# Optimization experiments

Measured on AMD Instinct MI355X. Metric: run time of the kernel, lower is better.

## Reference

```python
import jax, jax.numpy as jnp
import numpy as np

INPUT_SIZE = 416
NUM_CLASSES = 80
A = 3  # anchors per yolo layer
SS = [13, 26, 52]  # grid sizes (strides 32/16/8)
ANCHORS = [[(116, 90), (156, 198), (373, 326)],
           [(30, 61), (62, 45), (59, 119)],
           [(10, 13), (16, 30), (33, 23)]]
B, L = 16, 50


def _build_priors():
    boxes, cols, rows, pws, phs, szs = [], [], [], [], [], []
    for l, S in enumerate(SS):
        for i in range(S):
            for j in range(S):
                cx, cy = (j + 0.5) / S, (i + 0.5) / S
                for (aw, ah) in ANCHORS[l]:
                    w, h = aw / INPUT_SIZE, ah / INPUT_SIZE
                    boxes.append((cx - 0.5 * w, cy - 0.5 * h, w, h))
                    cols.append(j); rows.append(i)
                    pws.append(aw); phs.append(ah); szs.append(S)
    f = lambda a: np.asarray(a, np.float32)
    return f(boxes), f(cols), f(rows), f(pws), f(phs), f(szs)

PRIORS_NP, PCOL_NP, PROW_NP, PPW_NP, PPH_NP, PS_NP = _build_priors()
N = PRIORS_NP.shape[0]  # 10647
OFF = np.concatenate([[0], np.cumsum([S * S * A for S in SS])])


def setup_inputs() -> dict:
    key = jax.random.key(0)
    ks = jax.random.split(key, 8)
    inp = {}
    for l, S in enumerate(SS):
        inp[f"yolo_out{l}"] = jax.random.normal(ks[l], (B, A * (NUM_CLASSES + 5), S, S), jnp.float32)
    cls = jax.random.randint(ks[3], (B, L), 0, NUM_CLASSES).astype(jnp.float32)
    valid = jax.random.uniform(ks[4], (B, L)) < 0.4
    cls = jnp.where(valid, cls, -1.0)  # class < 0 means padding label
    xy = jax.random.uniform(ks[5], (B, L, 2), minval=0.0, maxval=0.7)
    wh = jax.random.uniform(ks[6], (B, L, 2), minval=0.05, maxval=0.3)
    inp["labels"] = jnp.concatenate([cls[..., None], xy, wh], axis=-1)[:, None]  # [B,1,L,5]
    return inp


def _bce(p, t):
    # torch BCELoss (mean) with the same log clamp at -100
    lg = lambda x: jnp.maximum(jnp.log(x), -100.0)
    return jnp.mean(-(t * lg(p) + (1.0 - t) * lg(1.0 - p)))


def _build_targets(labels):
    pri = jnp.asarray(PRIORS_NP)
    lab = labels[:, 0]  # [B,L,5]
    cls = lab[..., 0]
    valid = cls >= 0.0  # [B,L]
    bx, by, bw, bh = lab[..., 1], lab[..., 2], lab[..., 3], lab[..., 4]
    px, py, pw, ph = pri[:, 0], pri[:, 1], pri[:, 2], pri[:, 3]
    # IoU of every label against every prior: [B,L,N]
    ix = jnp.maximum(px, bx[..., None]); iy = jnp.maximum(py, by[..., None])
    ax = jnp.minimum(px + pw, (bx + bw)[..., None]); ay = jnp.minimum(py + ph, (by + bh)[..., None])
    inter = jnp.maximum(ax - ix, 0.0) * jnp.maximum(ay - iy, 0.0)
    ious = inter / (pw * ph + (bw * bh)[..., None] - inter)

    # priors with IoU>=0.5 to any gt are ignored for objectness (unless chosen as best)
    suppressed = jnp.any((ious >= 0.5) & valid[..., None], axis=1)  # [B,N]

    # best prior per label; on ties, pick the middle tied index (as the original)
    m = jnp.max(ious, axis=-1, keepdims=True)
    tie = ious == m
    k = tie.sum(-1)
    rank = (k - 1) // 2 + 1
    cs = jnp.cumsum(tie, -1)
    idx = jnp.argmax(tie & (cs == rank[..., None]), axis=-1)  # [B,L]

    colc = jnp.asarray(PCOL_NP)[idx]; rowc = jnp.asarray(PROW_NP)[idx]
    pwc = jnp.asarray(PPW_NP)[idx]; phc = jnp.asarray(PPH_NP)[idx]
    Sc = jnp.asarray(PS_NP)[idx]
    dx = jnp.clip((bx + 0.5 * bw) * Sc - colc, 1e-6, 0.999999)
    dy = jnp.clip((by + 0.5 * bh) * Sc - rowc, 1e-6, 0.999999)
    t_all = jnp.stack([jnp.log(dx / (1.0 - dx)), jnp.log(dy / (1.0 - dy)),
                       jnp.log(bw * INPUT_SIZE / pwc), jnp.log(bh * INPUT_SIZE / phc)], -1)  # [B,L,4]

    flat = (jnp.arange(B)[:, None] * N + idx).reshape(-1)  # [B*L]
    vflat = valid.reshape(-1)
    g = jnp.arange(B * L)
    winner = jax.ops.segment_max(jnp.where(vflat, g, -1), flat, num_segments=B * N)
    chosen = winner >= 0  # [B*N]
    coord_t = jnp.where(chosen[:, None], t_all.reshape(-1, 4)[jnp.clip(winner, 0)], 0.0)

    cls_i = jnp.where(vflat, cls.reshape(-1).astype(jnp.int32), 0)
    class_t = jnp.zeros((B * N, NUM_CLASSES), jnp.float32).at[flat, cls_i].max(vflat.astype(jnp.float32))

    obj_t = chosen.astype(jnp.float32).reshape(B, N)
    obj_m = (chosen.reshape(B, N) | ~suppressed).astype(jnp.float32)
    pos_m = chosen.astype(jnp.float32).reshape(B, N)
    return jax.lax.stop_gradient(
        (obj_t, obj_m, pos_m, coord_t.reshape(B, N, 4), class_t.reshape(B, N, NUM_CLASSES)))


def reference(yolo_out0, yolo_out1, yolo_out2, labels):
    obj_t, obj_m, pos_m, coord_t, class_t = _build_targets(labels)
    outs = [yolo_out0, yolo_out1, yolo_out2]
    Cp5 = NUM_CLASSES + 5
    obj_loss = coord_loss = class_loss = 0.0
    for l, S in enumerate(SS):
        n0, n1 = int(OFF[l]), int(OFF[l + 1])
        out = outs[l]
        # per-prior ordering within a layer is (row, col, anchor)
        om = obj_m[:, n0:n1].reshape(B, S, S, A).transpose(0, 3, 1, 2)
        ot = obj_t[:, n0:n1].reshape(B, S, S, A).transpose(0, 3, 1, 2)
        pm = pos_m[:, n0:n1].reshape(B, S, S, A)
        ct = coord_t[:, n0:n1].reshape(B, S, S, A, 4).transpose(0, 3, 4, 1, 2).reshape(B, A * 4, S, S)
        cm = jnp.broadcast_to(pm[..., None], (B, S, S, A, 4)).transpose(0, 3, 4, 1, 2).reshape(B, A * 4, S, S)
        kt = class_t[:, n0:n1].reshape(B, S, S, A, NUM_CLASSES).transpose(0, 3, 4, 1, 2).reshape(B, A * NUM_CLASSES, S, S)
        km = jnp.broadcast_to(pm[..., None], (B, S, S, A, NUM_CLASSES)).transpose(0, 3, 4, 1, 2).reshape(B, A * NUM_CLASSES, S, S)
        oi = np.arange(A) * Cp5 + 4
        ci = (np.arange(A)[:, None] * Cp5 + np.arange(4)).reshape(-1)
        ki = (np.arange(A)[:, None] * Cp5 + 5 + np.arange(NUM_CLASSES)).reshape(-1)
        obj_loss = obj_loss + _bce(jax.nn.sigmoid(out[:, oi]) * om, ot * om)
        coord_loss = coord_loss + jnp.mean((out[:, ci] * cm - ct * cm) ** 2)
        class_loss = class_loss + _bce(jax.nn.sigmoid(out[:, ki]) * km, kt * km)
    return jnp.stack([obj_loss, coord_loss, class_loss])
```

## Files before the change

### kernel.cpp

```cpp
#include <hip/hip_runtime.h>

#define NPRI 10647
#define BB 16
#define LL 50
#define OBJ_BLOCKS 666
#define CHO_BLOCKS (BB * LL)
#define TOT_BLOCKS (OBJ_BLOCKS + CHO_BLOCKS)

__device__ __constant__ double c_hw[3][3] = {
    {0.5*(116.0/416.0), 0.5*(156.0/416.0), 0.5*(373.0/416.0)},
    {0.5*( 30.0/416.0), 0.5*( 62.0/416.0), 0.5*( 59.0/416.0)},
    {0.5*( 10.0/416.0), 0.5*( 16.0/416.0), 0.5*( 33.0/416.0)}};
__device__ __constant__ double c_hh[3][3] = {
    {0.5*( 90.0/416.0), 0.5*(198.0/416.0), 0.5*(326.0/416.0)},
    {0.5*( 61.0/416.0), 0.5*( 45.0/416.0), 0.5*(119.0/416.0)},
    {0.5*( 23.0/416.0), 0.5*( 30.0/416.0), 0.5*( 23.0/416.0)}};
__device__ __constant__ float c_pwf[3][3] = {
    {(float)(116.0/416.0), (float)(156.0/416.0), (float)(373.0/416.0)},
    {(float)( 30.0/416.0), (float)( 62.0/416.0), (float)( 59.0/416.0)},
    {(float)( 10.0/416.0), (float)( 16.0/416.0), (float)( 33.0/416.0)}};
__device__ __constant__ float c_phf[3][3] = {
    {(float)( 90.0/416.0), (float)(198.0/416.0), (float)(326.0/416.0)},
    {(float)( 61.0/416.0), (float)( 45.0/416.0), (float)(119.0/416.0)},
    {(float)( 23.0/416.0), (float)( 30.0/416.0), (float)( 23.0/416.0)}};
__device__ __constant__ float c_awf[3][3] = {{116,156,373},{30,62,59},{10,16,33}};
__device__ __constant__ float c_ahf[3][3] = {{90,198,326},{61,45,119},{23,30,23}};
__device__ __constant__ double c_wObj[3] = {1.0/8112.0, 1.0/32448.0, 1.0/129792.0};

__device__ inline void decode_prior(int n, int& level, int& S, int& ii, int& jj,
                                    int& aa, int& off) {
    if (n < 507)        { level = 0; S = 13; int c = n / 3;            aa = n - 3*c;            jj = c % 13; ii = c / 13; off = 0;  }
    else if (n < 2535)  { level = 1; S = 26; int nn = n - 507;  int c = nn / 3; aa = nn - 3*c; jj = c % 26; ii = c / 26; off = 13; }
    else                { level = 2; S = 52; int nn = n - 2535; int c = nn / 3; aa = nn - 3*c; jj = c % 52; ii = c / 52; off = 39; }
}

__global__ __launch_bounds__(256) void assign_kernel(
    const float* __restrict__ labels, int* __restrict__ idxArr,
    float4* __restrict__ tcoord) {
    __shared__ double s_cx[91];
    __shared__ float  s_iou[NPRI];
    __shared__ float  s_red[256];
    __shared__ int    s_cnt[256];

    int tid = threadIdx.x;
    int gi  = blockIdx.x;
    const float* lab = labels + gi * 5;
    float cls = lab[0];
    if (tid == 0) idxArr[gi] = -1;
    if (cls < 0.0f) return;

    if (tid < 91) {
        int S, idx;
        if (tid < 13)      { S = 13; idx = tid; }
        else if (tid < 39) { S = 26; idx = tid - 13; }
        else               { S = 52; idx = tid - 39; }
        s_cx[tid] = ((double)idx + 0.5) / (double)S;
    }

    float bx = lab[1], by = lab[2], bw = lab[3], bh = lab[4];
    float bxe  = __fadd_rn(bx, bw), bye = __fadd_rn(by, bh);
    float bwbh = __fmul_rn(bw, bh);
    __syncthreads();

    float lmax = -3.0e38f;
    for (int n = tid; n < NPRI; n += 256) {
        int level, S, ii, jj, aa, off;
        decode_prior(n, level, S, ii, jj, aa, off);
        float px  = (float)(s_cx[off + jj] - c_hw[level][aa]);
        float py  = (float)(s_cx[off + ii] - c_hh[level][aa]);
        float pwf = c_pwf[level][aa], phf = c_phf[level][aa];
        float pxe = __fadd_rn(px, pwf), pye = __fadd_rn(py, phf);
        float pwph = __fmul_rn(pwf, phf);
        float ix = fmaxf(px, bx), iy = fmaxf(py, by);
        float ax = fminf(pxe, bxe), ay = fminf(pye, bye);
        float iw = fmaxf(__fsub_rn(ax, ix), 0.0f);
        float ih = fmaxf(__fsub_rn(ay, iy), 0.0f);
        float inter = __fmul_rn(iw, ih);
        float denom = __fsub_rn(__fadd_rn(pwph, bwbh), inter);
        float iou = __fdiv_rn(inter, denom);
        s_iou[n] = iou;
        lmax = fmaxf(lmax, iou);
    }
    s_red[tid] = lmax;
    __syncthreads();
    for (int s = 128; s > 0; s >>= 1) {
        if (tid < s) s_red[tid] = fmaxf(s_red[tid], s_red[tid + s]);
        __syncthreads();
    }
    float m = s_red[0];

    const int CH = 42;
    int start = tid * CH;
    int end   = min(start + CH, NPRI);
    int cnt = 0;
    for (int n = start; n < end; ++n) cnt += (s_iou[n] == m) ? 1 : 0;

    s_cnt[tid] = cnt;
    __syncthreads();
    for (int d = 1; d < 256; d <<= 1) {
        int add = (tid >= d) ? s_cnt[tid - d] : 0;
        __syncthreads();
        s_cnt[tid] += add;
        __syncthreads();
    }
    int k    = s_cnt[255];
    int rank = (k - 1) / 2 + 1;
    int pre  = s_cnt[tid] - cnt;

    if (pre < rank && rank <= pre + cnt) {
        int r = rank - pre;
        int sel = -1;
        for (int n = start; n < end; ++n)
            if (s_iou[n] == m && --r == 0) { sel = n; break; }
        int level, S, ii, jj, aa, off;
        decode_prior(sel, level, S, ii, jj, aa, off);
        float Sf = (float)S, colf = (float)jj, rowf = (float)ii;
        float dx = __fsub_rn(__fmul_rn(__fadd_rn(bx, __fmul_rn(0.5f, bw)), Sf), colf);
        float dy = __fsub_rn(__fmul_rn(__fadd_rn(by, __fmul_rn(0.5f, bh)), Sf), rowf);
        dx = fminf(fmaxf(dx, 1e-6f), 0.999999f);
        dy = fminf(fmaxf(dy, 1e-6f), 0.999999f);
        float t0 = logf(__fdiv_rn(dx, __fsub_rn(1.0f, dx)));
        float t1 = logf(__fdiv_rn(dy, __fsub_rn(1.0f, dy)));
        float t2 = logf(__fdiv_rn(__fmul_rn(bw, 416.0f), c_awf[level][aa]));
        float t3 = logf(__fdiv_rn(__fmul_rn(bh, 416.0f), c_ahf[level][aa]));
        tcoord[gi] = make_float4(t0, t1, t2, t3);
        idxArr[gi] = sel;
    }
}

__global__ __launch_bounds__(256) void loss_kernel(
    const float* __restrict__ o0, const float* __restrict__ o1, const float* __restrict__ o2,
    const float* __restrict__ labels, const int* __restrict__ idxArr,
    const float4* __restrict__ tcoord,
    double* __restrict__ pObj, double* __restrict__ pCoord, double* __restrict__ pClass) {
    __shared__ float  s_box[2][LL][4];
    __shared__ float  s_cls[2][LL];
    __shared__ int    s_idx[2][LL];
    __shared__ double s_red[256];
    int tid = threadIdx.x;

    if (blockIdx.x < OBJ_BLOCKS) {
        int e0 = blockIdx.x * 256;
        int b0 = e0 / NPRI;
        int b1 = min((e0 + 255) / NPRI, BB - 1);
        for (int t = tid; t < 2 * LL; t += 256) {
            int which = t / LL, l = t - which * LL;
            int b = which ? b1 : b0;
            const float* lab = labels + (b * LL + l) * 5;
            s_cls[which][l]    = lab[0];
            s_box[which][l][0] = lab[1];
            s_box[which][l][1] = lab[2];
            s_box[which][l][2] = lab[3];
            s_box[which][l][3] = lab[4];
            s_idx[which][l]    = idxArr[b * LL + l];
        }
        __syncthreads();

        int e = e0 + tid;
        double a = 0.0;
        if (e < BB * NPRI) {
            int b = e / NPRI, n = e - b * NPRI;
            int which = (b == b0) ? 0 : 1;
            int level, S, ii, jj, aa, off;
            decode_prior(n, level, S, ii, jj, aa, off);
            double cxd = ((double)jj + 0.5) / (double)S;
            double cyd = ((double)ii + 0.5) / (double)S;
            float px  = (float)(cxd - c_hw[level][aa]);
            float py  = (float)(cyd - c_hh[level][aa]);
            float pwf = c_pwf[level][aa], phf = c_phf[level][aa];
            float pxe = __fadd_rn(px, pwf), pye = __fadd_rn(py, phf);
            float pwph = __fmul_rn(pwf, phf);
            bool supp = false, chosen = false;
            for (int l = 0; l < LL; ++l) {
                if (s_cls[which][l] < 0.0f) continue;
                if (s_idx[which][l] == n) chosen = true;
                float bx = s_box[which][l][0], by = s_box[which][l][1];
                float bw = s_box[which][l][2], bh = s_box[which][l][3];
                float ix = fmaxf(px, bx), iy = fmaxf(py, by);
                float ax = fminf(pxe, __fadd_rn(bx, bw));
                float ay = fminf(pye, __fadd_rn(by, bh));
                float iw = fmaxf(__fsub_rn(ax, ix), 0.0f);
                float ih = fmaxf(__fsub_rn(ay, iy), 0.0f);
                float inter = __fmul_rn(iw, ih);
                float denom = __fsub_rn(__fadd_rn(pwph, __fmul_rn(bw, bh)), inter);
                float iou = __fdiv_rn(inter, denom);
                if (iou >= 0.5f) supp = true;
            }
            if (chosen || !supp) {
                int SS2 = S * S;
                const float* out = (level == 0) ? o0 : ((level == 1) ? o1 : o2);
                float x = out[(size_t)b * 255 * SS2 + (aa * 85 + 4) * SS2 + ii * S + jj];
                float p = 1.0f / (1.0f + expf(-x));
                float t = chosen ? 1.0f : 0.0f;
                float lp = fmaxf(logf(p), -100.0f);
                float lq = fmaxf(logf(1.0f - p), -100.0f);
                a = -(double)(t * lp + (1.0f - t) * lq) * c_wObj[level];
            }
        }
        s_red[tid] = a; __syncthreads();
        for (int s = 128; s > 0; s >>= 1) { if (tid < s) s_red[tid] += s_red[tid + s]; __syncthreads(); }
        if (tid == 0) pObj[blockIdx.x] = s_red[0];
    } else {
        int gi = blockIdx.x - OBJ_BLOCKS;
        int b  = gi / LL, lsel = gi - b * LL;
        if (tid < LL) {
            s_idx[0][tid] = idxArr[b * LL + tid];
            s_cls[0][tid] = labels[(b * LL + tid) * 5];
        }
        __syncthreads();
        int sel = s_idx[0][lsel];
        int maxl = -1;
        if (sel >= 0)
            for (int l = 0; l < LL; ++l) if (s_idx[0][l] == sel) maxl = l;
        bool active = (sel >= 0) && (maxl == lsel);
        if (!active) {
            if (tid == 0) { pCoord[gi] = 0.0; pClass[gi] = 0.0; }
            return;
        }
        int level, S, ii, jj, aa, off;
        decode_prior(sel, level, S, ii, jj, aa, off);
        int SS2 = S * S;
        const float* out = (level == 0) ? o0 : ((level == 1) ? o1 : o2);
        const float* base = out + (size_t)b * 255 * SS2 + aa * 85 * SS2 + ii * S + jj;
        double wObj = c_wObj[level];

        double val = 0.0;
        if (tid < 4) {
            float4 ct = tcoord[gi];
            float ctk = (tid == 0) ? ct.x : (tid == 1) ? ct.y : (tid == 2) ? ct.z : ct.w;
            float x = base[tid * SS2];
            float d = __fsub_rn(x, ctk);
            val = (double)__fmul_rn(d, d) * (wObj * 0.25);
        } else if (tid >= 5 && tid < 85) {
            int cc = tid - 5;
            float x = base[tid * SS2];
            float t = 0.0f;
            for (int l = 0; l < LL; ++l)
                if (s_idx[0][l] == sel && (int)s_cls[0][l] == cc) t = 1.0f;
            float p = 1.0f / (1.0f + expf(-x));
            float lp = fmaxf(logf(p), -100.0f);
            float lq = fmaxf(logf(1.0f - p), -100.0f);
            val = -(double)(t * lp + (1.0f - t) * lq) * (wObj * 0.0125);
        }
        s_red[tid] = (tid < 4) ? val : 0.0;
        __syncthreads();
        for (int s = 128; s > 0; s >>= 1) { if (tid < s) s_red[tid] += s_red[tid + s]; __syncthreads(); }
        if (tid == 0) pCoord[gi] = s_red[0];
        __syncthreads();
        s_red[tid] = (tid >= 5 && tid < 85) ? val : 0.0;
        __syncthreads();
        for (int s = 128; s > 0; s >>= 1) { if (tid < s) s_red[tid] += s_red[tid + s]; __syncthreads(); }
        if (tid == 0) pClass[gi] = s_red[0];
    }
}

__global__ __launch_bounds__(256) void finalize_kernel(
    const double* __restrict__ pObj, const double* __restrict__ pCoord,
    const double* __restrict__ pClass, float* __restrict__ out) {
    int tid = threadIdx.x;
    double sO = 0.0, sC = 0.0, sK = 0.0;
    for (int i = tid; i < OBJ_BLOCKS; i += 256) sO += pObj[i];
    for (int i = tid; i < CHO_BLOCKS; i += 256) { sC += pCoord[i]; sK += pClass[i]; }
    __shared__ double r0[256], r1[256], r2[256];
    r0[tid] = sO; r1[tid] = sC; r2[tid] = sK;
    __syncthreads();
    for (int s = 128; s > 0; s >>= 1) {
        if (tid < s) { r0[tid] += r0[tid + s]; r1[tid] += r1[tid + s]; r2[tid] += r2[tid + s]; }
        __syncthreads();
    }
    if (tid == 0) { out[0] = (float)r0[0]; out[1] = (float)r1[0]; out[2] = (float)r2[0]; }
}

extern "C" void kernel_launch(void* const* d_in, const int* in_sizes, int n_in,
                              void* d_out, int out_size, void* d_ws, size_t ws_size,
                              hipStream_t stream) {
    const float* o0     = (const float*)d_in[0];
    const float* o1     = (const float*)d_in[1];
    const float* o2     = (const float*)d_in[2];
    const float* labels = (const float*)d_in[3];

    char* ws = (char*)d_ws;
    int*    idxArr = (int*)   (ws);
    float4* tcoord = (float4*)(ws + 3200);
    double* pObj   = (double*)(ws + 16000);
    double* pCoord = (double*)(ws + 21328);
    double* pClass = (double*)(ws + 27728);

    assign_kernel<<<BB * LL, 256, 0, stream>>>(labels, idxArr, tcoord);
    loss_kernel<<<TOT_BLOCKS, 256, 0, stream>>>(o0, o1, o2, labels, idxArr, tcoord,
                                                pObj, pCoord, pClass);
    finalize_kernel<<<1, 256, 0, stream>>>(pObj, pCoord, pClass, (float*)d_out);
}
```

Baseline: 127.0 us.

## Fuse finalize into loss kernel via last-block counter and compact valid labels

Removes the separate finalize launch by having the last block of the loss kernel, detected with an atomic counter and threadfence, perform the final reduction. The assign kernel's block reductions and scan now use wave shuffles instead of shared-memory loops with many barriers. The objectness path compacts valid labels with a ballot, precomputes box edges and areas, and replaces the per-pair IoU division with a double-precision threshold comparison. The added atomic and fences cost a little, and the division-free test relies on an exact constant to reproduce the original rounding.

Measured after the change: 154.5 us. +21.7%, slower.

```diff
diff --git a/kernel.cpp b/kernel.cpp
--- a/kernel.cpp
+++ b/kernel.cpp
@@ -6,6 +6,8 @@
 #define OBJ_BLOCKS 666
 #define CHO_BLOCKS (BB * LL)
 #define TOT_BLOCKS (OBJ_BLOCKS + CHO_BLOCKS)
+
+#define SUPP_C 0.49999998509883880615234375
 
 __device__ __constant__ double c_hw[3][3] = {
     {0.5*(116.0/416.0), 0.5*(156.0/416.0), 0.5*(373.0/416.0)},
@@ -36,14 +38,15 @@
 
 __global__ __launch_bounds__(256) void assign_kernel(
     const float* __restrict__ labels, int* __restrict__ idxArr,
-    float4* __restrict__ tcoord) {
+    float4* __restrict__ tcoord, int* __restrict__ counter) {
     __shared__ double s_cx[91];
     __shared__ float  s_iou[NPRI];
-    __shared__ float  s_red[256];
-    __shared__ int    s_cnt[256];
-
-    int tid = threadIdx.x;
+    __shared__ float  s_w[4];
+    __shared__ int    s_wsum[4];
+
+    int tid = threadIdx.x, lane = tid & 63, wid = tid >> 6;
     int gi  = blockIdx.x;
+    if (gi == 0 && tid == 0) *counter = 0;
     const float* lab = labels + gi * 5;
     float cls = lab[0];
     if (tid == 0) idxArr[gi] = -1;
@@ -81,13 +84,10 @@
         s_iou[n] = iou;
         lmax = fmaxf(lmax, iou);
     }
-    s_red[tid] = lmax;
+    for (int d = 1; d < 64; d <<= 1) lmax = fmaxf(lmax, __shfl_xor(lmax, d));
+    if (lane == 0) s_w[wid] = lmax;
     __syncthreads();
-    for (int s = 128; s > 0; s >>= 1) {
-        if (tid < s) s_red[tid] = fmaxf(s_red[tid], s_red[tid + s]);
-        __syncthreads();
-    }
-    float m = s_red[0];
+    float m = fmaxf(fmaxf(s_w[0], s_w[1]), fmaxf(s_w[2], s_w[3]));
 
     const int CH = 42;
     int start = tid * CH;
@@ -95,17 +95,17 @@
     int cnt = 0;
     for (int n = start; n < end; ++n) cnt += (s_iou[n] == m) ? 1 : 0;
 
-    s_cnt[tid] = cnt;
+    int incl = cnt;
+    for (int d = 1; d < 64; d <<= 1) {
+        int v = __shfl_up(incl, d);
+        if (lane >= d) incl += v;
+    }
+    if (lane == 63) s_wsum[wid] = incl;
     __syncthreads();
-    for (int d = 1; d < 256; d <<= 1) {
-        int add = (tid >= d) ? s_cnt[tid - d] : 0;
-        __syncthreads();
-        s_cnt[tid] += add;
-        __syncthreads();
-    }
-    int k    = s_cnt[255];
+    int woff = 0, k = 0;
+    for (int w = 0; w < 4; ++w) { int v = s_wsum[w]; k += v; if (w < wid) woff += v; }
     int rank = (k - 1) / 2 + 1;
-    int pre  = s_cnt[tid] - cnt;
+    int pre  = woff + incl - cnt;
 
     if (pre < rank && rank <= pre + cnt) {
         int r = rank - pre;
@@ -132,27 +132,47 @@
     const float* __restrict__ o0, const float* __restrict__ o1, const float* __restrict__ o2,
     const float* __restrict__ labels, const int* __restrict__ idxArr,
     const float4* __restrict__ tcoord,
-    double* __restrict__ pObj, double* __restrict__ pCoord, double* __restrict__ pClass) {
-    __shared__ float  s_box[2][LL][4];
-    __shared__ float  s_cls[2][LL];
-    __shared__ int    s_idx[2][LL];
+    double* __restrict__ pObj, double* __restrict__ pCoord, double* __restrict__ pClass,
+    int* __restrict__ counter, float* __restrict__ out) {
+    __shared__ double s_cx[91];
+    __shared__ float  s_lbx[2][LL], s_lby[2][LL], s_lxe[2][LL], s_lye[2][LL], s_lar[2][LL];
+    __shared__ int    s_lidx[2][LL];
+    __shared__ int    s_lcnt[2];
     __shared__ double s_red[256];
-    int tid = threadIdx.x;
+    __shared__ int    s_last;
+    int tid = threadIdx.x, lane = tid & 63, wid = tid >> 6;
 
     if (blockIdx.x < OBJ_BLOCKS) {
         int e0 = blockIdx.x * 256;
         int b0 = e0 / NPRI;
         int b1 = min((e0 + 255) / NPRI, BB - 1);
-        for (int t = tid; t < 2 * LL; t += 256) {
-            int which = t / LL, l = t - which * LL;
-            int b = which ? b1 : b0;
-            const float* lab = labels + (b * LL + l) * 5;
-            s_cls[which][l]    = lab[0];
-            s_box[which][l][0] = lab[1];
-            s_box[which][l][1] = lab[2];
-            s_box[which][l][2] = lab[3];
-            s_box[which][l][3] = lab[4];
-            s_idx[which][l]    = idxArr[b * LL + l];
+        if (tid < 91) {
+            int S, idx;
+            if (tid < 13)      { S = 13; idx = tid; }
+            else if (tid < 39) { S = 26; idx = tid - 13; }
+            else               { S = 52; idx = tid - 39; }
+            s_cx[tid] = ((double)idx + 0.5) / (double)S;
+        }
+        if (wid < 2) {
+            int b = wid ? b1 : b0;
+            float cls = -1.0f, bx = 0, by = 0, bw = 0, bh = 0; int idx = -1;
+            if (lane < LL) {
+                const float* lab = labels + (b * LL + lane) * 5;
+                cls = lab[0]; bx = lab[1]; by = lab[2]; bw = lab[3]; bh = lab[4];
+                idx = idxArr[b * LL + lane];
+            }
+            bool valid = (lane < LL) && (cls >= 0.0f);
+            unsigned long long mask = __ballot(valid);
+            if (valid) {
+                int pos = __popcll(mask & ((1ull << lane) - 1ull));
+                s_lbx[wid][pos] = bx;
+                s_lby[wid][pos] = by;
+                s_lxe[wid][pos] = __fadd_rn(bx, bw);
+                s_lye[wid][pos] = __fadd_rn(by, bh);
+                s_lar[wid][pos] = __fmul_rn(bw, bh);
+                s_lidx[wid][pos] = idx;
+            }
+            if (lane == 0) s_lcnt[wid] = __popcll(mask);
         }
         __syncthreads();
 
@@ -163,33 +183,29 @@
             int which = (b == b0) ? 0 : 1;
             int level, S, ii, jj, aa, off;
             decode_prior(n, level, S, ii, jj, aa, off);
-            double cxd = ((double)jj + 0.5) / (double)S;
-            double cyd = ((double)ii + 0.5) / (double)S;
-            float px  = (float)(cxd - c_hw[level][aa]);
-            float py  = (float)(cyd - c_hh[level][aa]);
+            float px  = (float)(s_cx[off + jj] - c_hw[level][aa]);
+            float py  = (float)(s_cx[off + ii] - c_hh[level][aa]);
             float pwf = c_pwf[level][aa], phf = c_phf[level][aa];
             float pxe = __fadd_rn(px, pwf), pye = __fadd_rn(py, phf);
             float pwph = __fmul_rn(pwf, phf);
             bool supp = false, chosen = false;
-            for (int l = 0; l < LL; ++l) {
-                if (s_cls[which][l] < 0.0f) continue;
-                if (s_idx[which][l] == n) chosen = true;
-                float bx = s_box[which][l][0], by = s_box[which][l][1];
-                float bw = s_box[which][l][2], bh = s_box[which][l][3];
-                float ix = fmaxf(px, bx), iy = fmaxf(py, by);
-                float ax = fminf(pxe, __fadd_rn(bx, bw));
-                float ay = fminf(pye, __fadd_rn(by, bh));
+            int cnt = s_lcnt[which];
+            for (int l = 0; l < cnt; ++l) {
+                chosen = chosen | (s_lidx[which][l] == n);
+                float ix = fmaxf(px, s_lbx[which][l]);
+                float iy = fmaxf(py, s_lby[which][l]);
+                float ax = fminf(pxe, s_lxe[which][l]);
+                float ay = fminf(pye, s_lye[which][l]);
                 float iw = fmaxf(__fsub_rn(ax, ix), 0.0f);
                 float ih = fmaxf(__fsub_rn(ay, iy), 0.0f);
                 float inter = __fmul_rn(iw, ih);
-                float denom = __fsub_rn(__fadd_rn(pwph, __fmul_rn(bw, bh)), inter);
-                float iou = __fdiv_rn(inter, denom);
-                if (iou >= 0.5f) supp = true;
+                float denom = __fsub_rn(__fadd_rn(pwph, s_lar[which][l]), inter);
+                supp = supp | ((double)inter >= SUPP_C * (double)denom);
             }
             if (chosen || !supp) {
                 int SS2 = S * S;
-                const float* out = (level == 0) ? o0 : ((level == 1) ? o1 : o2);
-                float x = out[(size_t)b * 255 * SS2 + (aa * 85 + 4) * SS2 + ii * S + jj];
+                const float* outp = (level == 0) ? o0 : ((level == 1) ? o1 : o2);
+                float x = outp[(size_t)b * 255 * SS2 + (aa * 85 + 4) * SS2 + ii * S + jj];
                 float p = 1.0f / (1.0f + expf(-x));
                 float t = chosen ? 1.0f : 0.0f;
                 float lp = fmaxf(logf(p), -100.0f);
@@ -204,71 +220,74 @@
         int gi = blockIdx.x - OBJ_BLOCKS;
         int b  = gi / LL, lsel = gi - b * LL;
         if (tid < LL) {
-            s_idx[0][tid] = idxArr[b * LL + tid];
-            s_cls[0][tid] = labels[(b * LL + tid) * 5];
-        }
-        __syncthreads();
-        int sel = s_idx[0][lsel];
+            s_lidx[0][tid] = idxArr[b * LL + tid];
+            s_lar[0][tid]  = labels[(b * LL + tid) * 5];
+        }
+        __syncthreads();
+        int sel = s_lidx[0][lsel];
         int maxl = -1;
         if (sel >= 0)
-            for (int l = 0; l < LL; ++l) if (s_idx[0][l] == sel) maxl = l;
+            for (int l = 0; l < LL; ++l) if (s_lidx[0][l] == sel) maxl = l;
         bool active = (sel >= 0) && (maxl == lsel);
-        if (!active) {
-            if (tid == 0) { pCoord[gi] = 0.0; pClass[gi] = 0.0; }
-            return;
-        }
-        int level, S, ii, jj, aa, off;
-        decode_prior(sel, level, S, ii, jj, aa, off);
-        int SS2 = S * S;
-        const float* out = (level == 0) ? o0 : ((level == 1) ? o1 : o2);
-        const float* base = out + (size_t)b * 255 * SS2 + aa * 85 * SS2 + ii * S + jj;
-        double wObj = c_wObj[level];
-
-        double val = 0.0;
-        if (tid < 4) {
-            float4 ct = tcoord[gi];
-            float ctk = (tid == 0) ? ct.x : (tid == 1) ? ct.y : (tid == 2) ? ct.z : ct.w;
-            float x = base[tid * SS2];
-            float d = __fsub_rn(x, ctk);
-            val = (double)__fmul_rn(d, d) * (wObj * 0.25);
-        } else if (tid >= 5 && tid < 85) {
-            int cc = tid - 5;
-            float x = base[tid * SS2];
-            float t = 0.0f;
-            for (int l = 0; l < LL; ++l)
-                if (s_idx[0][l] == sel && (int)s_cls[0][l] == cc) t = 1.0f;
-            float p = 1.0f / (1.0f + expf(-x));
-            float lp = fmaxf(logf(p), -100.0f);
-            float lq = fmaxf(logf(1.0f - p), -100.0f);
-            val = -(double)(t * lp + (1.0f - t) * lq) * (wObj * 0.0125);
-        }
-        s_red[tid] = (tid < 4) ? val : 0.0;
-        __syncthreads();
+
+        double vc = 0.0, vk = 0.0;
+        if (active) {
+            int level, S, ii, jj, aa, off;
+            decode_prior(sel, level, S, ii, jj, aa, off);
+            int SS2 = S * S;
+            const float* outp = (level == 0) ? o0 : ((level == 1) ? o1 : o2);
+            const float* base = outp + (size_t)b * 255 * SS2 + aa * 85 * SS2 + ii * S + jj;
+            double wObj = c_wObj[level];
+            if (tid < 4) {
+                float4 ct = tcoord[gi];
+                float ctk = (tid == 0) ? ct.x : (tid == 1) ? ct.y : (tid == 2) ? ct.z : ct.w;
+                float x = base[tid * SS2];
+                float d = __fsub_rn(x, ctk);
+                vc = (double)__fmul_rn(d, d) * (wObj * 0.25);
+            } else if (tid >= 5 && tid < 85) {
+                int cc = tid - 5;
+                float x = base[tid * SS2];
+                float t = 0.0f;
+                for (int l = 0; l < LL; ++l)
+                    if (s_lidx[0][l] == sel && (int)s_lar[0][l] == cc) t = 1.0f;
+                float p = 1.0f / (1.0f + expf(-x));
+                float lp = fmaxf(logf(p), -100.0f);
+                float lq = fmaxf(logf(1.0f - p), -100.0f);
+                vk = -(double)(t * lp + (1.0f - t) * lq) * (wObj * 0.0125);
+            }
+        }
+        s_red[tid] = vc; __syncthreads();
         for (int s = 128; s > 0; s >>= 1) { if (tid < s) s_red[tid] += s_red[tid + s]; __syncthreads(); }
         if (tid == 0) pCoord[gi] = s_red[0];
         __syncthreads();
-        s_red[tid] = (tid >= 5 && tid < 85) ? val : 0.0;
-        __syncthreads();
+        s_red[tid] = vk; __syncthreads();
         for (int s = 128; s > 0; s >>= 1) { if (tid < s) s_red[tid] += s_red[tid + s]; __syncthreads(); }
         if (tid == 0) pClass[gi] = s_red[0];
     }
-}
-
-__global__ __launch_bounds__(256) void finalize_kernel(
-    const double* __restrict__ pObj, const double* __restrict__ pCoord,
-    const double* __restrict__ pClass, float* __restrict__ out) {
-    int tid = threadIdx.x;
-    double sO = 0.0, sC = 0.0, sK = 0.0;
-    for (int i = tid; i < OBJ_BLOCKS; i += 256) sO += pObj[i];
-    for (int i = tid; i < CHO_BLOCKS; i += 256) { sC += pCoord[i]; sK += pClass[i]; }
-    __shared__ double r0[256], r1[256], r2[256];
-    r0[tid] = sO; r1[tid] = sC; r2[tid] = sK;
+
+    if (tid == 0) {
+        __threadfence();
+        int t = atomicAdd(counter, 1);
+        s_last = (t == TOT_BLOCKS - 1) ? 1 : 0;
+    }
     __syncthreads();
-    for (int s = 128; s > 0; s >>= 1) {
-        if (tid < s) { r0[tid] += r0[tid + s]; r1[tid] += r1[tid + s]; r2[tid] += r2[tid + s]; }
-        __syncthreads();
-    }
-    if (tid == 0) { out[0] = (float)r0[0]; out[1] = (float)r1[0]; out[2] = (float)r2[0]; }
+    if (s_last) {
+        __threadfence();
+        double sO = 0.0, sC = 0.0, sK = 0.0;
+        for (int i = tid; i < OBJ_BLOCKS; i += 256) sO += pObj[i];
+        for (int i = tid; i < CHO_BLOCKS; i += 256) { sC += pCoord[i]; sK += pClass[i]; }
+        s_red[tid] = sO; __syncthreads();
+        for (int s = 128; s > 0; s >>= 1) { if (tid < s) s_red[tid] += s_red[tid + s]; __syncthreads(); }
+        if (tid == 0) out[0] = (float)s_red[0];
+        __syncthreads();
+        s_red[tid] = sC; __syncthreads();
+        for (int s = 128; s > 0; s >>= 1) { if (tid < s) s_red[tid] += s_red[tid + s]; __syncthreads(); }
+        if (tid == 0) out[1] = (float)s_red[0];
+        __syncthreads();
+        s_red[tid] = sK; __syncthreads();
+        for (int s = 128; s > 0; s >>= 1) { if (tid < s) s_red[tid] += s_red[tid + s]; __syncthreads(); }
+        if (tid == 0) out[2] = (float)s_red[0];
+    }
 }
 
 extern "C" void kernel_launch(void* const* d_in, const int* in_sizes, int n_in,
@@ -280,14 +299,15 @@
     const float* labels = (const float*)d_in[3];
 
     char* ws = (char*)d_ws;
-    int*    idxArr = (int*)   (ws);
-    float4* tcoord = (float4*)(ws + 3200);
-    double* pObj   = (double*)(ws + 16000);
-    double* pCoord = (double*)(ws + 21328);
-    double* pClass = (double*)(ws + 27728);
-
-    assign_kernel<<<BB * LL, 256, 0, stream>>>(labels, idxArr, tcoord);
+    int*    idxArr  = (int*)   (ws);
+    float4* tcoord  = (float4*)(ws + 3200);
+    double* pObj    = (double*)(ws + 16000);
+    double* pCoord  = (double*)(ws + 21328);
+    double* pClass  = (double*)(ws + 27728);
+    int*    counter = (int*)   (ws + 34128);
+
+    assign_kernel<<<BB * LL, 256, 0, stream>>>(labels, idxArr, tcoord, counter);
     loss_kernel<<<TOT_BLOCKS, 256, 0, stream>>>(o0, o1, o2, labels, idxArr, tcoord,
-                                                pObj, pCoord, pClass);
-    finalize_kernel<<<1, 256, 0, stream>>>(pObj, pCoord, pClass, (float*)d_out);
+                                                pObj, pCoord, pClass, counter,
+                                                (float*)d_out);
 }
```

## Remap objectness blocks per (batch, anchor, level) and compact valid labels

Applied to the files above, without the earlier changes.

Objectness blocks are re-indexed so each block covers one batch/anchor pair at one level, which makes the objectness logit loads contiguous and removes the per-element prior decode. Valid labels are compacted with a ballot into shared arrays, with box ends and areas precomputed, so the IoU loop runs only over real labels. The IoU division is replaced by a double-precision multiply against a threshold constant. The block count and workspace offsets change to match, and the double comparison could in principle differ from the float division at boundary cases.

New measurement: 124.8 us. No clear change (-1.7%).

```diff
diff --git a/kernel.cpp b/kernel.cpp
--- a/kernel.cpp
+++ b/kernel.cpp
@@ -3,9 +3,11 @@
 #define NPRI 10647
 #define BB 16
 #define LL 50
-#define OBJ_BLOCKS 666
+#define OBJ_BLOCKS 720
 #define CHO_BLOCKS (BB * LL)
 #define TOT_BLOCKS (OBJ_BLOCKS + CHO_BLOCKS)
+
+#define SUPP_C 0.49999998509883880615234375
 
 __device__ __constant__ double c_hw[3][3] = {
     {0.5*(116.0/416.0), 0.5*(156.0/416.0), 0.5*(373.0/416.0)},
@@ -133,63 +135,75 @@
     const float* __restrict__ labels, const int* __restrict__ idxArr,
     const float4* __restrict__ tcoord,
     double* __restrict__ pObj, double* __restrict__ pCoord, double* __restrict__ pClass) {
-    __shared__ float  s_box[2][LL][4];
-    __shared__ float  s_cls[2][LL];
-    __shared__ int    s_idx[2][LL];
+    __shared__ double s_cx[52];
+    __shared__ float  s_lbx[LL], s_lby[LL], s_lxe[LL], s_lye[LL], s_lar[LL];
+    __shared__ int    s_lidx[LL];
+    __shared__ int    s_lcnt;
+    __shared__ int    s_cidx[LL];
+    __shared__ float  s_ccls[LL];
     __shared__ double s_red[256];
-    int tid = threadIdx.x;
+    int tid = threadIdx.x, lane = tid & 63, wid = tid >> 6;
 
     if (blockIdx.x < OBJ_BLOCKS) {
-        int e0 = blockIdx.x * 256;
-        int b0 = e0 / NPRI;
-        int b1 = min((e0 + 255) / NPRI, BB - 1);
-        for (int t = tid; t < 2 * LL; t += 256) {
-            int which = t / LL, l = t - which * LL;
-            int b = which ? b1 : b0;
-            const float* lab = labels + (b * LL + l) * 5;
-            s_cls[which][l]    = lab[0];
-            s_box[which][l][0] = lab[1];
-            s_box[which][l][1] = lab[2];
-            s_box[which][l][2] = lab[3];
-            s_box[which][l][3] = lab[4];
-            s_idx[which][l]    = idxArr[b * LL + l];
+        int bid = blockIdx.x;
+        int level, m, chunk, S, SS2, lvloff;
+        if (bid < 48)       { level = 0; m = bid;        chunk = 0;          S = 13; SS2 = 169;  lvloff = 0;    }
+        else if (bid < 192) { level = 1; int q = bid-48; m = q / 3;  chunk = q - 3*m + 0;  S = 26; SS2 = 676;  lvloff = 507;
+                              chunk = (q - 3*m); }
+        else                { level = 2; int q = bid-192; m = q / 11; chunk = q - 11*m;    S = 52; SS2 = 2704; lvloff = 2535; }
+        int b  = m / 3;
+        int aa = m - 3 * b;
+        int pos = chunk * 256 + tid;
+
+        if (tid < S) s_cx[tid] = ((double)tid + 0.5) / (double)S;
+        if (wid == 0) {
+            float cls = -1.0f, lbx = 0, lby = 0, lbw = 0, lbh = 0; int idx = -1;
+            if (lane < LL) {
+                const float* lab = labels + (b * LL + lane) * 5;
+                cls = lab[0]; lbx = lab[1]; lby = lab[2]; lbw = lab[3]; lbh = lab[4];
+                idx = idxArr[b * LL + lane];
+            }
+            bool valid = (lane < LL) && (cls >= 0.0f);
+            unsigned long long mask = __ballot(valid);
+            if (valid) {
+                int p = __popcll(mask & ((1ull << lane) - 1ull));
+                s_lbx[p] = lbx;
+                s_lby[p] = lby;
+                s_lxe[p] = __fadd_rn(lbx, lbw);
+                s_lye[p] = __fadd_rn(lby, lbh);
+                s_lar[p] = __fmul_rn(lbw, lbh);
+                s_lidx[p] = idx;
+            }
+            if (lane == 0) s_lcnt = __popcll(mask);
         }
         __syncthreads();
 
-        int e = e0 + tid;
         double a = 0.0;
-        if (e < BB * NPRI) {
-            int b = e / NPRI, n = e - b * NPRI;
-            int which = (b == b0) ? 0 : 1;
-            int level, S, ii, jj, aa, off;
-            decode_prior(n, level, S, ii, jj, aa, off);
-            double cxd = ((double)jj + 0.5) / (double)S;
-            double cyd = ((double)ii + 0.5) / (double)S;
-            float px  = (float)(cxd - c_hw[level][aa]);
-            float py  = (float)(cyd - c_hh[level][aa]);
+        if (pos < SS2) {
+            const float* outp = (level == 0) ? o0 : ((level == 1) ? o1 : o2);
+            float x = outp[((size_t)b * 255 + aa * 85 + 4) * SS2 + pos];
+            int ii = pos / S, jj = pos - ii * S;
+            int n  = lvloff + pos * 3 + aa;
+            float px  = (float)(s_cx[jj] - c_hw[level][aa]);
+            float py  = (float)(s_cx[ii] - c_hh[level][aa]);
             float pwf = c_pwf[level][aa], phf = c_phf[level][aa];
             float pxe = __fadd_rn(px, pwf), pye = __fadd_rn(py, phf);
             float pwph = __fmul_rn(pwf, phf);
             bool supp = false, chosen = false;
-            for (int l = 0; l < LL; ++l) {
-                if (s_cls[which][l] < 0.0f) continue;
-                if (s_idx[which][l] == n) chosen = true;
-                float bx = s_box[which][l][0], by = s_box[which][l][1];
-                float bw = s_box[which][l][2], bh = s_box[which][l][3];
-                float ix = fmaxf(px, bx), iy = fmaxf(py, by);
-                float ax = fminf(pxe, __fadd_rn(bx, bw));
-                float ay = fminf(pye, __fadd_rn(by, bh));
+            int cnt = s_lcnt;
+            for (int l = 0; l < cnt; ++l) {
+                chosen = chosen | (s_lidx[l] == n);
+                float ix = fmaxf(px, s_lbx[l]);
+                float iy = fmaxf(py, s_lby[l]);
+                float ax = fminf(pxe, s_lxe[l]);
+                float ay = fminf(pye, s_lye[l]);
                 float iw = fmaxf(__fsub_rn(ax, ix), 0.0f);
                 float ih = fmaxf(__fsub_rn(ay, iy), 0.0f);
                 float inter = __fmul_rn(iw, ih);
-                float denom = __fsub_rn(__fadd_rn(pwph, __fmul_rn(bw, bh)), inter);
-                float iou = __fdiv_rn(inter, denom);
-                if (iou >= 0.5f) supp = true;
+                float denom = __fsub_rn(__fadd_rn(pwph, s_lar[l]), inter);
+                supp = supp | ((double)inter >= SUPP_C * (double)denom);
             }
             if (chosen || !supp) {
-                int SS2 = S * S;
-                const float* out = (level == 0) ? o0 : ((level == 1) ? o1 : o2);
-                float x = out[(size_t)b * 255 * SS2 + (aa * 85 + 4) * SS2 + ii * S + jj];
                 float p = 1.0f / (1.0f + expf(-x));
                 float t = chosen ? 1.0f : 0.0f;
                 float lp = fmaxf(logf(p), -100.0f);
@@ -199,56 +213,52 @@
         }
         s_red[tid] = a; __syncthreads();
         for (int s = 128; s > 0; s >>= 1) { if (tid < s) s_red[tid] += s_red[tid + s]; __syncthreads(); }
-        if (tid == 0) pObj[blockIdx.x] = s_red[0];
+        if (tid == 0) pObj[bid] = s_red[0];
     } else {
         int gi = blockIdx.x - OBJ_BLOCKS;
         int b  = gi / LL, lsel = gi - b * LL;
         if (tid < LL) {
-            s_idx[0][tid] = idxArr[b * LL + tid];
-            s_cls[0][tid] = labels[(b * LL + tid) * 5];
+            s_cidx[tid] = idxArr[b * LL + tid];
+            s_ccls[tid] = labels[(b * LL + tid) * 5];
         }
         __syncthreads();
-        int sel = s_idx[0][lsel];
+        int sel = s_cidx[lsel];
         int maxl = -1;
         if (sel >= 0)
-            for (int l = 0; l < LL; ++l) if (s_idx[0][l] == sel) maxl = l;
+            for (int l = 0; l < LL; ++l) if (s_cidx[l] == sel) maxl = l;
         bool active = (sel >= 0) && (maxl == lsel);
-        if (!active) {
-            if (tid == 0) { pCoord[gi] = 0.0; pClass[gi] = 0.0; }
-            return;
+
+        double vc = 0.0, vk = 0.0;
+        if (active) {
+            int level, S, ii, jj, aa, off;
+            decode_prior(sel, level, S, ii, jj, aa, off);
+            int SS2 = S * S;
+            const float* outp = (level == 0) ? o0 : ((level == 1) ? o1 : o2);
+            const float* base = outp + (size_t)b * 255 * SS2 + aa * 85 * SS2 + ii * S + jj;
+            double wObj = c_wObj[level];
+            if (tid < 4) {
+                float4 ct = tcoord[gi];
+                float ctk = (tid == 0) ? ct.x : (tid == 1) ? ct.y : (tid == 2) ? ct.z : ct.w;
+                float x = base[tid * SS2];
+                float d = __fsub_rn(x, ctk);
+                vc = (double)__fmul_rn(d, d) * (wObj * 0.25);
+            } else if (tid >= 5 && tid < 85) {
+                int cc = tid - 5;
+                float x = base[tid * SS2];
+                float t = 0.0f;
+                for (int l = 0; l < LL; ++l)
+                    if (s_cidx[l] == sel && (int)s_ccls[l] == cc) t = 1.0f;
+                float p = 1.0f / (1.0f + expf(-x));
+                float lp = fmaxf(logf(p), -100.0f);
+                float lq = fmaxf(logf(1.0f - p), -100.0f);
+                vk = -(double)(t * lp + (1.0f - t) * lq) * (wObj * 0.0125);
+            }
         }
-        int level, S, ii, jj, aa, off;
-        decode_prior(sel, level, S, ii, jj, aa, off);
-        int SS2 = S * S;
-        const float* out = (level == 0) ? o0 : ((level == 1) ? o1 : o2);
-        const float* base = out + (size_t)b * 255 * SS2 + aa * 85 * SS2 + ii * S + jj;
-        double wObj = c_wObj[level];
-
-        double val = 0.0;
-        if (tid < 4) {
-            float4 ct = tcoord[gi];
-            float ctk = (tid == 0) ? ct.x : (tid == 1) ? ct.y : (tid == 2) ? ct.z : ct.w;
-            float x = base[tid * SS2];
-            float d = __fsub_rn(x, ctk);
-            val = (double)__fmul_rn(d, d) * (wObj * 0.25);
-        } else if (tid >= 5 && tid < 85) {
-            int cc = tid - 5;
-            float x = base[tid * SS2];
-            float t = 0.0f;
-            for (int l = 0; l < LL; ++l)
-                if (s_idx[0][l] == sel && (int)s_cls[0][l] == cc) t = 1.0f;
-            float p = 1.0f / (1.0f + expf(-x));
-            float lp = fmaxf(logf(p), -100.0f);
-            float lq = fmaxf(logf(1.0f - p), -100.0f);
-            val = -(double)(t * lp + (1.0f - t) * lq) * (wObj * 0.0125);
-        }
-        s_red[tid] = (tid < 4) ? val : 0.0;
-        __syncthreads();
+        s_red[tid] = vc; __syncthreads();
         for (int s = 128; s > 0; s >>= 1) { if (tid < s) s_red[tid] += s_red[tid + s]; __syncthreads(); }
         if (tid == 0) pCoord[gi] = s_red[0];
         __syncthreads();
-        s_red[tid] = (tid >= 5 && tid < 85) ? val : 0.0;
-        __syncthreads();
+        s_red[tid] = vk; __syncthreads();
         for (int s = 128; s > 0; s >>= 1) { if (tid < s) s_red[tid] += s_red[tid + s]; __syncthreads(); }
         if (tid == 0) pClass[gi] = s_red[0];
     }
@@ -283,8 +293,8 @@
     int*    idxArr = (int*)   (ws);
     float4* tcoord = (float4*)(ws + 3200);
     double* pObj   = (double*)(ws + 16000);
-    double* pCoord = (double*)(ws + 21328);
-    double* pClass = (double*)(ws + 27728);
+    double* pCoord = (double*)(ws + 21760);
+    double* pClass = (double*)(ws + 28160);
 
     assign_kernel<<<BB * LL, 256, 0, stream>>>(labels, idxArr, tcoord);
     loss_kernel<<<TOT_BLOCKS, 256, 0, stream>>>(o0, o1, o2, labels, idxArr, tcoord,
```
